# Kernel tuning notes

Hardware: AMD Instinct MI355X
Metric: run time of the kernel (lower is better)

The kernel has to match this reference:

```python
import jax, jax.numpy as jnp
import numpy as np

B, T, D, H, L = 256, 1024, 64, 128, 2

def _lstm_layer(x, h0, c0, w_ih, w_hh, b):
    # x: [B,T,Din]; w_ih: [4H,Din]; w_hh: [4H,H]; b: [4H]
    xg = jnp.einsum('btd,gd->btg', x, w_ih) + b  # precompute input-to-gate GEMM: [B,T,4H]
    def step(carry, xt):
        h, c = carry
        g = xt + h @ w_hh.T                       # [B,4H], torch gate order i,f,g,o
        i, f, gg, o = jnp.split(g, 4, axis=-1)
        c = jax.nn.sigmoid(f) * c + jax.nn.sigmoid(i) * jnp.tanh(gg)
        h = jax.nn.sigmoid(o) * jnp.tanh(c)
        return (h, c), h
    _, hs = jax.lax.scan(step, (h0, c0), jnp.swapaxes(xg, 0, 1))  # hs: [T,B,H]
    return jnp.swapaxes(hs, 0, 1)


def setup_inputs() -> dict:
    key = jax.random.key(0)
    ks = jax.random.split(key, 12)
    s = 1.0 / np.sqrt(H)
    u = lambda k, shp: jax.random.uniform(k, shp, jnp.float32, -s, s)
    return {
        'x': jax.random.normal(ks[0], (B, T, D), jnp.float32),
        'h0': jax.random.normal(ks[1], (L, B, H), jnp.float32),
        'w_ih_0': u(ks[2], (4 * H, D)),
        'w_hh_0': u(ks[3], (4 * H, H)),
        'b_0': u(ks[4], (4 * H,)),
        'w_ih_1': u(ks[5], (4 * H, H)),
        'w_hh_1': u(ks[6], (4 * H, H)),
        'b_1': u(ks[7], (4 * H,)),
        'fc_w': u(ks[8], (1, H)),
        'fc_b': u(ks[9], (1,)),
    }


def reference(x, h0, w_ih_0, w_hh_0, b_0, w_ih_1, w_hh_1, b_1, fc_w, fc_b):
    c0 = jnp.zeros((x.shape[0], w_hh_0.shape[1]), x.dtype)  # c0 = zeros as in original
    h = _lstm_layer(x, h0[0], c0, w_ih_0, w_hh_0, b_0)
    h = _lstm_layer(h, h0[1], c0, w_ih_1, w_hh_1, b_1)
    return h[:, -1, :] @ fc_w.T + fc_b  # fc2 on last timestep -> [B,1]
```

## Files before the change

### kernel.cpp

```cpp
#include <hip/hip_runtime.h>
#include <math.h>

#define NB  256
#define T   1024
#define DIN 64
#define H   128
#define G4  512

typedef __attribute__((ext_vector_type(8))) short    bf16x8;
typedef __attribute__((ext_vector_type(4))) float    f32x4;
typedef __attribute__((ext_vector_type(8))) _Float16 f16x8;

#define DPPQ(v, CTRL) __int_as_float(__builtin_amdgcn_update_dpp(0, __float_as_int(v), (CTRL), 0xf, 0xf, true))

__device__ __forceinline__ float sigf(float x)   { return 1.0f / (1.0f + __expf(-x)); }
__device__ __forceinline__ float tanhf_(float x) { return 2.0f / (1.0f + __expf(-2.0f * x)) - 1.0f; }

__device__ __forceinline__ void split_bf16(float x, short& hi, short& lo) {
    unsigned u = __float_as_uint(x);
    unsigned hb = (u + 0x7fffu + ((u >> 16) & 1u)) >> 16;
    hi = (short)hb;
    float r = x - __uint_as_float(hb << 16);
    unsigned u2 = __float_as_uint(r);
    lo = (short)((u2 + 0x7fffu + ((u2 >> 16) & 1u)) >> 16);
}

struct SJ {
    const _Float16* xg;
    const float* whh;
    const float* bias;
    const float* h0;
    float* sth; float* stc;
    short* hh; short* hl;
    int first;
    int dofc;
};

template<int TILE>
__global__ __launch_bounds__(512, 4)
void scan2(SJ ja, SJ jb, int nbA,
           const float* __restrict__ fcw, const float* __restrict__ fcb,
           float* __restrict__ out)
{
    __shared__ _Float16 __align__(16) lds_h[2][H];
    __shared__ float lds_r[H];

    const int bid = blockIdx.x;
    const bool isA = bid < nbA;
    const SJ J = isA ? ja : jb;
    const int b = isA ? bid : bid - nbA;

    const int t    = threadIdx.x;
    const int lane = t & 63;
    const int w    = t >> 6;
    const int kg   = t & 3;
    const int hu   = t >> 2;
    const int kt_grp = lane >> 4;

    f16x8 wfrag[4][4];
    #pragma unroll
    for (int j = 0; j < 4; ++j) {
        const int n  = 64 * w + 16 * j + (lane & 15);
        const int pn = (n & 3) * 128 + (n >> 2);
        const float* wr = J.whh + (size_t)pn * H;
        #pragma unroll
        for (int kt = 0; kt < 4; ++kt) {
            const int base = 32 * kt + kt_grp * 8;
            float4 v0 = *(const float4*)(wr + base);
            float4 v1 = *(const float4*)(wr + base + 4);
            wfrag[j][kt] = (f16x8){(_Float16)v0.x, (_Float16)v0.y, (_Float16)v0.z, (_Float16)v0.w,
                                   (_Float16)v1.x, (_Float16)v1.y, (_Float16)v1.z, (_Float16)v1.w};
        }
    }
    const float bj = J.bias[kg * 128 + hu];

    const bool  isg = (kg == 2);
    const float nsc = isg ? -2.0f : -1.0f;
    const float va  = isg ?  2.0f :  1.0f;
    const float vb  = isg ? -1.0f :  0.0f;

    if (t < H) {
        float hv = J.first ? J.h0[(size_t)b * H + t] : J.sth[(size_t)b * H + t];
        lds_h[0][t] = (_Float16)hv;
    }
    float c = J.first ? 0.0f : J.stc[(size_t)b * H + hu];
    __syncthreads();

    const _Float16* xgb = J.xg + (size_t)b * TILE * G4 + t;
    float xv0 = (float)xgb[0];
    float xv1 = (TILE > 1) ? (float)xgb[G4] : 0.0f;

    const bool s4 = (lane & 16) != 0;
    const bool s5 = (lane & 32) != 0;

    float hreg = 0.0f;
    int cur = 0;

    for (int tt = 0; tt < TILE; ++tt) {
        const _Float16* hb = &lds_h[cur][0];
        f16x8 af0 = *(const f16x8*)(hb +  0 + kt_grp * 8);
        f16x8 af1 = *(const f16x8*)(hb + 32 + kt_grp * 8);
        f16x8 af2 = *(const f16x8*)(hb + 64 + kt_grp * 8);
        f16x8 af3 = *(const f16x8*)(hb + 96 + kt_grp * 8);

        const f32x4 z = (f32x4){0.f, 0.f, 0.f, 0.f};
        f32x4 a0 = __builtin_amdgcn_mfma_f32_16x16x32_f16(af0, wfrag[0][0], z, 0, 0, 0);
        f32x4 a1 = __builtin_amdgcn_mfma_f32_16x16x32_f16(af0, wfrag[1][0], z, 0, 0, 0);
        f32x4 a2 = __builtin_amdgcn_mfma_f32_16x16x32_f16(af0, wfrag[2][0], z, 0, 0, 0);
        f32x4 a3 = __builtin_amdgcn_mfma_f32_16x16x32_f16(af0, wfrag[3][0], z, 0, 0, 0);
        f32x4 b0 = __builtin_amdgcn_mfma_f32_16x16x32_f16(af2, wfrag[0][2], z, 0, 0, 0);
        f32x4 b1 = __builtin_amdgcn_mfma_f32_16x16x32_f16(af2, wfrag[1][2], z, 0, 0, 0);
        f32x4 b2 = __builtin_amdgcn_mfma_f32_16x16x32_f16(af2, wfrag[2][2], z, 0, 0, 0);
        f32x4 b3 = __builtin_amdgcn_mfma_f32_16x16x32_f16(af2, wfrag[3][2], z, 0, 0, 0);
        a0 = __builtin_amdgcn_mfma_f32_16x16x32_f16(af1, wfrag[0][1], a0, 0, 0, 0);
        a1 = __builtin_amdgcn_mfma_f32_16x16x32_f16(af1, wfrag[1][1], a1, 0, 0, 0);
        a2 = __builtin_amdgcn_mfma_f32_16x16x32_f16(af1, wfrag[2][1], a2, 0, 0, 0);
        a3 = __builtin_amdgcn_mfma_f32_16x16x32_f16(af1, wfrag[3][1], a3, 0, 0, 0);
        b0 = __builtin_amdgcn_mfma_f32_16x16x32_f16(af3, wfrag[0][3], b0, 0, 0, 0);
        b1 = __builtin_amdgcn_mfma_f32_16x16x32_f16(af3, wfrag[1][3], b1, 0, 0, 0);
        b2 = __builtin_amdgcn_mfma_f32_16x16x32_f16(af3, wfrag[2][3], b2, 0, 0, 0);
        b3 = __builtin_amdgcn_mfma_f32_16x16x32_f16(af3, wfrag[3][3], b3, 0, 0, 0);

        float gloA = s4 ? a1[0] : a0[0];
        float ghiA = s4 ? a3[0] : a2[0];
        float gloB = s4 ? b1[0] : b0[0];
        float ghiB = s4 ? b3[0] : b2[0];
        float g = (s5 ? ghiA : gloA) + (s5 ? ghiB : gloB) + xv0 + bj;

        xv0 = xv1;
        int tn = (tt + 2 < TILE) ? (tt + 2) : (TILE - 1);
        xv1 = (float)xgb[(size_t)tn * G4];

        float u  = 1.0f / (1.0f + __expf(nsc * g));
        float vl = fmaf(u, va, vb);

        float ni = DPPQ(vl, 0x00);
        float nf = DPPQ(vl, 0x55);
        float ng = DPPQ(vl, 0xAA);
        float no = DPPQ(vl, 0xFF);

        c = nf * c + ni * ng;
        float h = no * tanhf_(c);
        hreg = h;

        if (kg == 0) {
            lds_h[cur ^ 1][hu] = (_Float16)h;
            if (J.hh) {
                short hs, ls; split_bf16(h, hs, ls);
                size_t ix = ((size_t)b * TILE + tt) * H + hu;
                J.hh[ix] = hs; J.hl[ix] = ls;
            }
        }
        cur ^= 1;
        __syncthreads();
    }

    if (kg == 0) {
        J.sth[(size_t)b * H + hu] = hreg;
        J.stc[(size_t)b * H + hu] = c;
    }

    if (J.dofc) {
        if (kg == 0) lds_r[hu] = hreg * fcw[hu];
        __syncthreads();
        if (t == 0) {
            float s = fcb[0];
            for (int k = 0; k < H; ++k) s += lds_r[k];
            out[b] = s;
        }
    }
}

__global__ __launch_bounds__(256)
void prep(const float* __restrict__ x,
          const float* __restrict__ wih0, const float* __restrict__ wih1,
          short* __restrict__ Xh, short* __restrict__ Xl,
          short* __restrict__ W0h, short* __restrict__ W0l,
          short* __restrict__ W1h, short* __restrict__ W1l)
{
    const int NX4 = NB * T * DIN / 4;
    int gid = blockIdx.x * blockDim.x + threadIdx.x;
    int gs  = gridDim.x * blockDim.x;
    for (int i = gid; i < NX4; i += gs) {
        float4 v = ((const float4*)x)[i];
        short h0s, l0s, h1s, l1s, h2s, l2s, h3s, l3s;
        split_bf16(v.x, h0s, l0s); split_bf16(v.y, h1s, l1s);
        split_bf16(v.z, h2s, l2s); split_bf16(v.w, h3s, l3s);
        *(short4*)&Xh[4 * i] = make_short4(h0s, h1s, h2s, h3s);
        *(short4*)&Xl[4 * i] = make_short4(l0s, l1s, l2s, l3s);
    }
    for (int i = gid; i < 512 * 64; i += gs) {
        int np = i >> 6, k = i & 63;
        int pn = (np & 3) * 128 + (np >> 2);
        short hs, ls; split_bf16(wih0[pn * 64 + k], hs, ls);
        W0h[i] = hs; W0l[i] = ls;
    }
    for (int i = gid; i < 512 * 128; i += gs) {
        int np = i >> 7, k = i & 127;
        int pn = (np & 3) * 128 + (np >> 2);
        short hs, ls; split_bf16(wih1[pn * 128 + k], hs, ls);
        W1h[i] = hs; W1l[i] = ls;
    }
}

struct GJ {
    const short* Ah; const short* Al;
    const short* Wh; const short* Wl;
    _Float16* O;
    int K, Astride, t0;
};

__global__ __launch_bounds__(256, 2)
void gemm_xg(GJ ja, GJ jb, int nbA, int lgT, int lgM)
{
    __shared__ short sAh[128][72], sAl[128][72], sWh[128][72], sWl[128][72];

    int bid = blockIdx.x;
    const GJ J = (bid < nbA) ? ja : jb;
    if (bid >= nbA) bid -= nbA;

    const int Mmask = (1 << lgM) - 1;
    const int m0 = (bid & Mmask) << 7;
    const int n0 = (bid >> lgM) << 7;
    const int Tmask = (1 << lgT) - 1;

    const int j = threadIdx.x;
    const int lane = j & 63, wv = j >> 6;
    const int wm = wv >> 1, wn = wv & 1;
    const int q = lane >> 4, n16 = lane & 15;

    f32x4 acc[4][4];
    #pragma unroll
    for (int a = 0; a < 4; ++a)
        #pragma unroll
        for (int bq = 0; bq < 4; ++bq) acc[a][bq] = (f32x4){0.f, 0.f, 0.f, 0.f};

    const int npass = J.K >> 6;
    for (int kp = 0; kp < npass; ++kp) {
        #pragma unroll
        for (int it = 0; it < 4; ++it) {
            int c = j + it * 256;
            int r = c >> 3, kc = (c & 7) << 3;
            int gr = m0 + r;
            size_t arow = (size_t)(gr >> lgT) * J.Astride + J.t0 + (gr & Tmask);
            size_t aoff = arow * J.K + (size_t)kp * 64 + kc;
            *(bf16x8*)&sAh[r][kc] = *(const bf16x8*)(J.Ah + aoff);
            *(bf16x8*)&sAl[r][kc] = *(const bf16x8*)(J.Al + aoff);
            size_t woff = (size_t)(n0 + r) * J.K + (size_t)kp * 64 + kc;
            *(bf16x8*)&sWh[r][kc] = *(const bf16x8*)(J.Wh + woff);
            *(bf16x8*)&sWl[r][kc] = *(const bf16x8*)(J.Wl + woff);
        }
        __syncthreads();

        #pragma unroll
        for (int kt = 0; kt < 2; ++kt) {
            const int kk = kt * 32 + q * 8;
            bf16x8 ah[4], al[4];
            #pragma unroll
            for (int mt = 0; mt < 4; ++mt) {
                int row = wm * 64 + mt * 16 + n16;
                ah[mt] = *(const bf16x8*)&sAh[row][kk];
                al[mt] = *(const bf16x8*)&sAl[row][kk];
            }
            #pragma unroll
            for (int nt = 0; nt < 4; ++nt) {
                int col = wn * 64 + nt * 16 + n16;
                bf16x8 bh = *(const bf16x8*)&sWh[col][kk];
                bf16x8 bl = *(const bf16x8*)&sWl[col][kk];
                #pragma unroll
                for (int mt = 0; mt < 4; ++mt) {
                    acc[mt][nt] = __builtin_amdgcn_mfma_f32_16x16x32_bf16(ah[mt], bh, acc[mt][nt], 0, 0, 0);
                    acc[mt][nt] = __builtin_amdgcn_mfma_f32_16x16x32_bf16(al[mt], bh, acc[mt][nt], 0, 0, 0);
                    acc[mt][nt] = __builtin_amdgcn_mfma_f32_16x16x32_bf16(ah[mt], bl, acc[mt][nt], 0, 0, 0);
                }
            }
        }
        __syncthreads();
    }

    #pragma unroll
    for (int mt = 0; mt < 4; ++mt) {
        #pragma unroll
        for (int nt = 0; nt < 4; ++nt) {
            int row = m0 + wm * 64 + mt * 16 + q * 4;
            int col = n0 + wn * 64 + nt * 16 + n16;
            #pragma unroll
            for (int r = 0; r < 4; ++r)
                J.O[(size_t)(row + r) * G4 + col] = (_Float16)acc[mt][nt][r];
        }
    }
}

template<int TILE>
static void run_all(const float* x, const float* h0,
                    const float* wih0, const float* whh0, const float* b0,
                    const float* wih1, const float* whh1, const float* b1,
                    const float* fcw, const float* fcb, float* out,
                    void* d_ws, hipStream_t stream)
{
    const int n_t = T / TILE;
    const int lgT = __builtin_ctz(TILE);
    const int lgM = lgT + 1;
    const int nbJ = 8 * TILE;

    float*    st  = (float*)d_ws;
    _Float16* xg0 = (_Float16*)(st + 4 * NB * H);
    _Float16* xg1 = xg0 + (size_t)NB * TILE * G4;
    short*    hh  = (short*)(xg1 + (size_t)NB * TILE * G4);
    short*    hl  = hh + (size_t)NB * TILE * H;
    short*    Xh  = hl + (size_t)NB * TILE * H;
    short*    Xl  = Xh + (size_t)NB * T * DIN;
    short*    W0h = Xl + (size_t)NB * T * DIN;
    short*    W0l = W0h + 512 * 64;
    short*    W1h = W0l + 512 * 64;
    short*    W1l = W1h + 512 * 128;
    float *st_h0 = st, *st_c0 = st + NB * H, *st_h1 = st + 2 * NB * H, *st_c1 = st + 3 * NB * H;

    prep<<<2048, 256, 0, stream>>>(x, wih0, wih1, Xh, Xl, W0h, W0l, W1h, W1l);

    SJ l0, l1;
    l0.whh = whh0; l0.bias = b0; l0.h0 = h0;                  l0.sth = st_h0; l0.stc = st_c0;
    l0.xg = xg0;   l0.hh = hh;   l0.hl = hl;  l0.dofc = 0;
    l1.whh = whh1; l1.bias = b1; l1.h0 = h0 + (size_t)NB * H; l1.sth = st_h1; l1.stc = st_c1;
    l1.xg = xg1;   l1.hh = nullptr; l1.hl = nullptr;

    GJ g0; g0.Ah = Xh; g0.Al = Xl; g0.Wh = W0h; g0.Wl = W0l; g0.O = xg0; g0.K = DIN; g0.Astride = T;    g0.t0 = 0;
    GJ g1; g1.Ah = hh; g1.Al = hl; g1.Wh = W1h; g1.Wl = W1l; g1.O = xg1; g1.K = H;   g1.Astride = TILE; g1.t0 = 0;

    gemm_xg<<<nbJ, 256, 0, stream>>>(g0, g0, nbJ, lgT, lgM);
    l0.first = 1;
    scan2<TILE><<<NB, 512, 0, stream>>>(l0, l0, NB, fcw, fcb, out);

    for (int k = 0; k < n_t; ++k) {
        if (k + 1 < n_t) {
            GJ ga = g1;
            GJ gb = g0; gb.t0 = (k + 1) * TILE;
            gemm_xg<<<2 * nbJ, 256, 0, stream>>>(ga, gb, nbJ, lgT, lgM);
            l0.first = 0;
            l1.first = (k == 0);
            l1.dofc = 0;
            scan2<TILE><<<2 * NB, 512, 0, stream>>>(l0, l1, NB, fcw, fcb, out);
        } else {
            gemm_xg<<<nbJ, 256, 0, stream>>>(g1, g1, nbJ, lgT, lgM);
            l1.first = (k == 0);
            l1.dofc = 1;
            scan2<TILE><<<NB, 512, 0, stream>>>(l1, l1, NB, fcw, fcb, out);
        }
    }
}

extern "C" void kernel_launch(void* const* d_in, const int* in_sizes, int n_in,
                              void* d_out, int out_size, void* d_ws, size_t ws_size,
                              hipStream_t stream)
{
    const float* x    = (const float*)d_in[0];
    const float* h0   = (const float*)d_in[1];
    const float* wih0 = (const float*)d_in[2];
    const float* whh0 = (const float*)d_in[3];
    const float* b0   = (const float*)d_in[4];
    const float* wih1 = (const float*)d_in[5];
    const float* whh1 = (const float*)d_in[6];
    const float* b1   = (const float*)d_in[7];
    const float* fcw  = (const float*)d_in[8];
    const float* fcb  = (const float*)d_in[9];
    float* out = (float*)d_out;

    int TILE = 256;
    while (TILE > 16) {
        size_t need = (size_t)4 * NB * H * 4
                    + (size_t)NB * TILE * (2 * G4 * 2 + 2 * H * 2)
                    + (size_t)2 * NB * T * DIN * 2
                    + (size_t)2 * (512 * 64 + 512 * 128) * 2;
        if (need <= ws_size) break;
        TILE >>= 1;
    }

    switch (TILE) {
        case 256: run_all<256>(x, h0, wih0, whh0, b0, wih1, whh1, b1, fcw, fcb, out, d_ws, stream); break;
        case 128: run_all<128>(x, h0, wih0, whh0, b0, wih1, whh1, b1, fcw, fcb, out, d_ws, stream); break;
        case  64: run_all< 64>(x, h0, wih0, whh0, b0, wih1, whh1, b1, fcw, fcb, out, d_ws, stream); break;
        default:  run_all< 32>(x, h0, wih0, whh0, b0, wih1, whh1, b1, fcw, fcb, out, d_ws, stream); break;
    }
}
```

Before: 1.395 ms.

## Process four batch rows per scan block using MFMA row slots

The recurrent scan kernel now handles four batch rows per block instead of one, filling four of the MFMA's 16 M-rows with distinct sequences so each block does four times the useful work per step with the same weight fragments. This uses a quarter as many blocks (64 or 128 instead of 256 or 512), and each thread now computes its own h output, so every thread writes to LDS and global memory. The hidden-state hi/lo bf16 split is packed into one 32-bit word, and the GEMM unpacks it when loading. The cost is more per-thread gate work and fewer blocks to fill the GPU's compute units.

```diff
diff --git a/kernel.cpp b/kernel.cpp
--- a/kernel.cpp
+++ b/kernel.cpp
@@ -31,142 +31,167 @@
     const float* bias;
     const float* h0;
     float* sth; float* stc;
-    short* hh; short* hl;
+    unsigned* hp;
     int first;
     int dofc;
 };
 
 template<int TILE>
-__global__ __launch_bounds__(512, 4)
-void scan2(SJ ja, SJ jb, int nbA,
+__global__ __launch_bounds__(512, 2)
+void scan4(SJ ja, SJ jb, int nbA,
            const float* __restrict__ fcw, const float* __restrict__ fcb,
            float* __restrict__ out)
 {
-    __shared__ _Float16 __align__(16) lds_h[2][H];
-    __shared__ float lds_r[H];
+    __shared__ _Float16 __align__(16) lds_h[2][4][144];
+    __shared__ float lds_r[4][128];
 
     const int bid = blockIdx.x;
     const bool isA = bid < nbA;
     const SJ J = isA ? ja : jb;
-    const int b = isA ? bid : bid - nbA;
+    const int b0 = (isA ? bid : bid - nbA) << 2;
 
     const int t    = threadIdx.x;
     const int lane = t & 63;
     const int w    = t >> 6;
-    const int kg   = t & 3;
+    const int l15  = lane & 15;
+    const int q    = lane >> 4;
     const int hu   = t >> 2;
-    const int kt_grp = lane >> 4;
+    const int gg_  = t & 3;
+    const int rb   = lane & 3;
 
     f16x8 wfrag[4][4];
     #pragma unroll
     for (int j = 0; j < 4; ++j) {
-        const int n  = 64 * w + 16 * j + (lane & 15);
+        const int n  = 64 * w + 16 * j + l15;
         const int pn = (n & 3) * 128 + (n >> 2);
         const float* wr = J.whh + (size_t)pn * H;
         #pragma unroll
         for (int kt = 0; kt < 4; ++kt) {
-            const int base = 32 * kt + kt_grp * 8;
+            const int base = 32 * kt + q * 8;
             float4 v0 = *(const float4*)(wr + base);
             float4 v1 = *(const float4*)(wr + base + 4);
             wfrag[j][kt] = (f16x8){(_Float16)v0.x, (_Float16)v0.y, (_Float16)v0.z, (_Float16)v0.w,
                                    (_Float16)v1.x, (_Float16)v1.y, (_Float16)v1.z, (_Float16)v1.w};
         }
     }
-    const float bj = J.bias[kg * 128 + hu];
-
-    const bool  isg = (kg == 2);
+    const float bj = J.bias[gg_ * 128 + hu];
+
+    const bool  isg = (gg_ == 2);
     const float nsc = isg ? -2.0f : -1.0f;
     const float va  = isg ?  2.0f :  1.0f;
     const float vb  = isg ? -1.0f :  0.0f;
 
-    if (t < H) {
-        float hv = J.first ? J.h0[(size_t)b * H + t] : J.sth[(size_t)b * H + t];
-        lds_h[0][t] = (_Float16)hv;
-    }
-    float c = J.first ? 0.0f : J.stc[(size_t)b * H + hu];
+    {
+        int bb = t >> 7, hh_ = t & 127;
+        float hv = J.first ? J.h0[(size_t)(b0 + bb) * H + hh_]
+                           : J.sth[(size_t)(b0 + bb) * H + hh_];
+        lds_h[0][bb][hh_] = (_Float16)hv;
+    }
+    float c[4];
+    #pragma unroll
+    for (int r = 0; r < 4; ++r)
+        c[r] = J.first ? 0.0f : J.stc[(size_t)(b0 + r) * H + hu];
     __syncthreads();
 
-    const _Float16* xgb = J.xg + (size_t)b * TILE * G4 + t;
-    float xv0 = (float)xgb[0];
-    float xv1 = (TILE > 1) ? (float)xgb[G4] : 0.0f;
+    const _Float16* xgb = J.xg + (size_t)b0 * TILE * G4 + t;
+    float xv0[4], xv1[4];
+    #pragma unroll
+    for (int r = 0; r < 4; ++r) {
+        xv0[r] = (float)xgb[(size_t)r * TILE * G4];
+        xv1[r] = (TILE > 1) ? (float)xgb[(size_t)r * TILE * G4 + G4] : 0.0f;
+    }
 
     const bool s4 = (lane & 16) != 0;
     const bool s5 = (lane & 32) != 0;
-
-    float hreg = 0.0f;
+    const bool o1 = (lane & 1)  != 0;
+    const bool o2 = (lane & 2)  != 0;
+
+    float hreg = 0.0f, creg = 0.0f;
     int cur = 0;
 
     for (int tt = 0; tt < TILE; ++tt) {
-        const _Float16* hb = &lds_h[cur][0];
-        f16x8 af0 = *(const f16x8*)(hb +  0 + kt_grp * 8);
-        f16x8 af1 = *(const f16x8*)(hb + 32 + kt_grp * 8);
-        f16x8 af2 = *(const f16x8*)(hb + 64 + kt_grp * 8);
-        f16x8 af3 = *(const f16x8*)(hb + 96 + kt_grp * 8);
+        const _Float16* hb = &lds_h[cur][0][0];
+        const int ab = (l15 & 3) * 144 + q * 8;
+        f16x8 af0 = *(const f16x8*)(hb + ab +  0);
+        f16x8 af1 = *(const f16x8*)(hb + ab + 32);
+        f16x8 af2 = *(const f16x8*)(hb + ab + 64);
+        f16x8 af3 = *(const f16x8*)(hb + ab + 96);
 
         const f32x4 z = (f32x4){0.f, 0.f, 0.f, 0.f};
-        f32x4 a0 = __builtin_amdgcn_mfma_f32_16x16x32_f16(af0, wfrag[0][0], z, 0, 0, 0);
-        f32x4 a1 = __builtin_amdgcn_mfma_f32_16x16x32_f16(af0, wfrag[1][0], z, 0, 0, 0);
-        f32x4 a2 = __builtin_amdgcn_mfma_f32_16x16x32_f16(af0, wfrag[2][0], z, 0, 0, 0);
-        f32x4 a3 = __builtin_amdgcn_mfma_f32_16x16x32_f16(af0, wfrag[3][0], z, 0, 0, 0);
-        f32x4 b0 = __builtin_amdgcn_mfma_f32_16x16x32_f16(af2, wfrag[0][2], z, 0, 0, 0);
-        f32x4 b1 = __builtin_amdgcn_mfma_f32_16x16x32_f16(af2, wfrag[1][2], z, 0, 0, 0);
-        f32x4 b2 = __builtin_amdgcn_mfma_f32_16x16x32_f16(af2, wfrag[2][2], z, 0, 0, 0);
-        f32x4 b3 = __builtin_amdgcn_mfma_f32_16x16x32_f16(af2, wfrag[3][2], z, 0, 0, 0);
-        a0 = __builtin_amdgcn_mfma_f32_16x16x32_f16(af1, wfrag[0][1], a0, 0, 0, 0);
-        a1 = __builtin_amdgcn_mfma_f32_16x16x32_f16(af1, wfrag[1][1], a1, 0, 0, 0);
-        a2 = __builtin_amdgcn_mfma_f32_16x16x32_f16(af1, wfrag[2][1], a2, 0, 0, 0);
-        a3 = __builtin_amdgcn_mfma_f32_16x16x32_f16(af1, wfrag[3][1], a3, 0, 0, 0);
-        b0 = __builtin_amdgcn_mfma_f32_16x16x32_f16(af3, wfrag[0][3], b0, 0, 0, 0);
-        b1 = __builtin_amdgcn_mfma_f32_16x16x32_f16(af3, wfrag[1][3], b1, 0, 0, 0);
-        b2 = __builtin_amdgcn_mfma_f32_16x16x32_f16(af3, wfrag[2][3], b2, 0, 0, 0);
-        b3 = __builtin_amdgcn_mfma_f32_16x16x32_f16(af3, wfrag[3][3], b3, 0, 0, 0);
-
-        float gloA = s4 ? a1[0] : a0[0];
-        float ghiA = s4 ? a3[0] : a2[0];
-        float gloB = s4 ? b1[0] : b0[0];
-        float ghiB = s4 ? b3[0] : b2[0];
-        float g = (s5 ? ghiA : gloA) + (s5 ? ghiB : gloB) + xv0 + bj;
-
-        xv0 = xv1;
+        f32x4 aA0 = __builtin_amdgcn_mfma_f32_16x16x32_f16(af0, wfrag[0][0], z, 0, 0, 0);
+        f32x4 aA1 = __builtin_amdgcn_mfma_f32_16x16x32_f16(af0, wfrag[1][0], z, 0, 0, 0);
+        f32x4 aA2 = __builtin_amdgcn_mfma_f32_16x16x32_f16(af0, wfrag[2][0], z, 0, 0, 0);
+        f32x4 aA3 = __builtin_amdgcn_mfma_f32_16x16x32_f16(af0, wfrag[3][0], z, 0, 0, 0);
+        f32x4 aB0 = __builtin_amdgcn_mfma_f32_16x16x32_f16(af2, wfrag[0][2], z, 0, 0, 0);
+        f32x4 aB1 = __builtin_amdgcn_mfma_f32_16x16x32_f16(af2, wfrag[1][2], z, 0, 0, 0);
+        f32x4 aB2 = __builtin_amdgcn_mfma_f32_16x16x32_f16(af2, wfrag[2][2], z, 0, 0, 0);
+        f32x4 aB3 = __builtin_amdgcn_mfma_f32_16x16x32_f16(af2, wfrag[3][2], z, 0, 0, 0);
+        aA0 = __builtin_amdgcn_mfma_f32_16x16x32_f16(af1, wfrag[0][1], aA0, 0, 0, 0);
+        aA1 = __builtin_amdgcn_mfma_f32_16x16x32_f16(af1, wfrag[1][1], aA1, 0, 0, 0);
+        aA2 = __builtin_amdgcn_mfma_f32_16x16x32_f16(af1, wfrag[2][1], aA2, 0, 0, 0);
+        aA3 = __builtin_amdgcn_mfma_f32_16x16x32_f16(af1, wfrag[3][1], aA3, 0, 0, 0);
+        aB0 = __builtin_amdgcn_mfma_f32_16x16x32_f16(af3, wfrag[0][3], aB0, 0, 0, 0);
+        aB1 = __builtin_amdgcn_mfma_f32_16x16x32_f16(af3, wfrag[1][3], aB1, 0, 0, 0);
+        aB2 = __builtin_amdgcn_mfma_f32_16x16x32_f16(af3, wfrag[2][3], aB2, 0, 0, 0);
+        aB3 = __builtin_amdgcn_mfma_f32_16x16x32_f16(af3, wfrag[3][3], aB3, 0, 0, 0);
+
+        float g4[4];
+        #pragma unroll
+        for (int r = 0; r < 4; ++r) {
+            float vA = s5 ? (s4 ? aA3[r] : aA2[r]) : (s4 ? aA1[r] : aA0[r]);
+            float vB = s5 ? (s4 ? aB3[r] : aB2[r]) : (s4 ? aB1[r] : aB0[r]);
+            g4[r] = vA + vB + xv0[r] + bj;
+        }
+
         int tn = (tt + 2 < TILE) ? (tt + 2) : (TILE - 1);
-        xv1 = (float)xgb[(size_t)tn * G4];
-
-        float u  = 1.0f / (1.0f + __expf(nsc * g));
-        float vl = fmaf(u, va, vb);
-
-        float ni = DPPQ(vl, 0x00);
-        float nf = DPPQ(vl, 0x55);
-        float ng = DPPQ(vl, 0xAA);
-        float no = DPPQ(vl, 0xFF);
-
-        c = nf * c + ni * ng;
-        float h = no * tanhf_(c);
-        hreg = h;
-
-        if (kg == 0) {
-            lds_h[cur ^ 1][hu] = (_Float16)h;
-            if (J.hh) {
-                short hs, ls; split_bf16(h, hs, ls);
-                size_t ix = ((size_t)b * TILE + tt) * H + hu;
-                J.hh[ix] = hs; J.hl[ix] = ls;
-            }
+        #pragma unroll
+        for (int r = 0; r < 4; ++r) {
+            xv0[r] = xv1[r];
+            xv1[r] = (float)xgb[((size_t)r * TILE + tn) * G4];
+        }
+
+        float vl[4];
+        #pragma unroll
+        for (int r = 0; r < 4; ++r) {
+            float u = 1.0f / (1.0f + __expf(nsc * g4[r]));
+            vl[r] = fmaf(u, va, vb);
+        }
+
+        float no_[4];
+        #pragma unroll
+        for (int r = 0; r < 4; ++r) {
+            float ni = DPPQ(vl[r], 0x00);
+            float nf = DPPQ(vl[r], 0x55);
+            float ng = DPPQ(vl[r], 0xAA);
+            no_[r]   = DPPQ(vl[r], 0xFF);
+            c[r] = nf * c[r] + ni * ng;
+        }
+
+        float c_own  = o2 ? (o1 ? c[3]   : c[2])   : (o1 ? c[1]   : c[0]);
+        float no_own = o2 ? (o1 ? no_[3] : no_[2]) : (o1 ? no_[1] : no_[0]);
+        float h = no_own * tanhf_(c_own);
+        hreg = h; creg = c_own;
+
+        lds_h[cur ^ 1][rb][hu] = (_Float16)h;
+        if (J.hp) {
+            short hs, ls; split_bf16(h, hs, ls);
+            J.hp[((size_t)(b0 + rb) * TILE + tt) * H + hu] =
+                (unsigned)(unsigned short)hs | ((unsigned)(unsigned short)ls << 16);
         }
         cur ^= 1;
         __syncthreads();
     }
 
-    if (kg == 0) {
-        J.sth[(size_t)b * H + hu] = hreg;
-        J.stc[(size_t)b * H + hu] = c;
-    }
+    J.sth[(size_t)(b0 + rb) * H + hu] = hreg;
+    J.stc[(size_t)(b0 + rb) * H + hu] = creg;
 
     if (J.dofc) {
-        if (kg == 0) lds_r[hu] = hreg * fcw[hu];
+        lds_r[rb][hu] = hreg * fcw[hu];
         __syncthreads();
-        if (t == 0) {
+        if (t < 4) {
             float s = fcb[0];
-            for (int k = 0; k < H; ++k) s += lds_r[k];
-            out[b] = s;
+            for (int k = 0; k < H; ++k) s += lds_r[t][k];
+            out[b0 + t] = s;
         }
     }
 }
@@ -204,10 +229,10 @@
 }
 
 struct GJ {
-    const short* Ah; const short* Al;
+    const void* Ah; const void* Al;
     const short* Wh; const short* Wl;
     _Float16* O;
-    int K, Astride, t0;
+    int K, Astride, t0, apack;
 };
 
 __global__ __launch_bounds__(256, 2)
@@ -244,8 +269,26 @@
             int gr = m0 + r;
             size_t arow = (size_t)(gr >> lgT) * J.Astride + J.t0 + (gr & Tmask);
             size_t aoff = arow * J.K + (size_t)kp * 64 + kc;
-            *(bf16x8*)&sAh[r][kc] = *(const bf16x8*)(J.Ah + aoff);
-            *(bf16x8*)&sAl[r][kc] = *(const bf16x8*)(J.Al + aoff);
+            if (J.apack) {
+                const unsigned* ap = (const unsigned*)J.Ah;
+                uint4 p0 = *(const uint4*)(ap + aoff);
+                uint4 p1 = *(const uint4*)(ap + aoff + 4);
+                unsigned h01 = (p0.x & 0xffffu) | (p0.y << 16);
+                unsigned h23 = (p0.z & 0xffffu) | (p0.w << 16);
+                unsigned h45 = (p1.x & 0xffffu) | (p1.y << 16);
+                unsigned h67 = (p1.z & 0xffffu) | (p1.w << 16);
+                unsigned l01 = (p0.x >> 16) | (p0.y & 0xffff0000u);
+                unsigned l23 = (p0.z >> 16) | (p0.w & 0xffff0000u);
+                unsigned l45 = (p1.x >> 16) | (p1.y & 0xffff0000u);
+                unsigned l67 = (p1.z >> 16) | (p1.w & 0xffff0000u);
+                *(uint4*)&sAh[r][kc] = make_uint4(h01, h23, h45, h67);
+                *(uint4*)&sAl[r][kc] = make_uint4(l01, l23, l45, l67);
+            } else {
+                const short* ah = (const short*)J.Ah;
+                const short* al = (const short*)J.Al;
+                *(bf16x8*)&sAh[r][kc] = *(const bf16x8*)(ah + aoff);
+                *(bf16x8*)&sAl[r][kc] = *(const bf16x8*)(al + aoff);
+            }
             size_t woff = (size_t)(n0 + r) * J.K + (size_t)kp * 64 + kc;
             *(bf16x8*)&sWh[r][kc] = *(const bf16x8*)(J.Wh + woff);
             *(bf16x8*)&sWl[r][kc] = *(const bf16x8*)(J.Wl + woff);
@@ -302,13 +345,13 @@
     const int lgT = __builtin_ctz(TILE);
     const int lgM = lgT + 1;
     const int nbJ = 8 * TILE;
+    const int nbS = NB / 4;
 
     float*    st  = (float*)d_ws;
     _Float16* xg0 = (_Float16*)(st + 4 * NB * H);
     _Float16* xg1 = xg0 + (size_t)NB * TILE * G4;
-    short*    hh  = (short*)(xg1 + (size_t)NB * TILE * G4);
-    short*    hl  = hh + (size_t)NB * TILE * H;
-    short*    Xh  = hl + (size_t)NB * TILE * H;
+    unsigned* hp  = (unsigned*)(xg1 + (size_t)NB * TILE * G4);
+    short*    Xh  = (short*)(hp + (size_t)NB * TILE * H);
     short*    Xl  = Xh + (size_t)NB * T * DIN;
     short*    W0h = Xl + (size_t)NB * T * DIN;
     short*    W0l = W0h + 512 * 64;
@@ -320,16 +363,16 @@
 
     SJ l0, l1;
     l0.whh = whh0; l0.bias = b0; l0.h0 = h0;                  l0.sth = st_h0; l0.stc = st_c0;
-    l0.xg = xg0;   l0.hh = hh;   l0.hl = hl;  l0.dofc = 0;
+    l0.xg = xg0;   l0.hp = hp;   l0.dofc = 0;
     l1.whh = whh1; l1.bias = b1; l1.h0 = h0 + (size_t)NB * H; l1.sth = st_h1; l1.stc = st_c1;
-    l1.xg = xg1;   l1.hh = nullptr; l1.hl = nullptr;
-
-    GJ g0; g0.Ah = Xh; g0.Al = Xl; g0.Wh = W0h; g0.Wl = W0l; g0.O = xg0; g0.K = DIN; g0.Astride = T;    g0.t0 = 0;
-    GJ g1; g1.Ah = hh; g1.Al = hl; g1.Wh = W1h; g1.Wl = W1l; g1.O = xg1; g1.K = H;   g1.Astride = TILE; g1.t0 = 0;
+    l1.xg = xg1;   l1.hp = nullptr;
+
+    GJ g0; g0.Ah = Xh; g0.Al = Xl;      g0.Wh = W0h; g0.Wl = W0l; g0.O = xg0; g0.K = DIN; g0.Astride = T;    g0.t0 = 0; g0.apack = 0;
+    GJ g1; g1.Ah = hp; g1.Al = nullptr; g1.Wh = W1h; g1.Wl = W1l; g1.O = xg1; g1.K = H;   g1.Astride = TILE; g1.t0 = 0; g1.apack = 1;
 
     gemm_xg<<<nbJ, 256, 0, stream>>>(g0, g0, nbJ, lgT, lgM);
     l0.first = 1;
-    scan2<TILE><<<NB, 512, 0, stream>>>(l0, l0, NB, fcw, fcb, out);
+    scan4<TILE><<<nbS, 512, 0, stream>>>(l0, l0, nbS, fcw, fcb, out);
 
     for (int k = 0; k < n_t; ++k) {
         if (k + 1 < n_t) {
@@ -339,12 +382,12 @@
             l0.first = 0;
             l1.first = (k == 0);
             l1.dofc = 0;
-            scan2<TILE><<<2 * NB, 512, 0, stream>>>(l0, l1, NB, fcw, fcb, out);
+            scan4<TILE><<<2 * nbS, 512, 0, stream>>>(l0, l1, nbS, fcw, fcb, out);
         } else {
             gemm_xg<<<nbJ, 256, 0, stream>>>(g1, g1, nbJ, lgT, lgM);
             l1.first = (k == 0);
             l1.dofc = 1;
-            scan2<TILE><<<NB, 512, 0, stream>>>(l1, l1, NB, fcw, fcb, out);
+            scan4<TILE><<<nbS, 512, 0, stream>>>(l1, l1, nbS, fcw, fcb, out);
         }
     }
 }
@@ -368,7 +411,7 @@
     int TILE = 256;
     while (TILE > 16) {
         size_t need = (size_t)4 * NB * H * 4
-                    + (size_t)NB * TILE * (2 * G4 * 2 + 2 * H * 2)
+                    + (size_t)NB * TILE * (2 * G4 * 2 + H * 4)
                     + (size_t)2 * NB * T * DIN * 2
                     + (size_t)2 * (512 * 64 + 512 * 128) * 2;
         if (need <= ws_size) break;
```

Measured after the change: 1.639 ms. +17.5%, slower.
